# Kernel optimization log

Measured on AMD Instinct MI355X. Metric: run time of the kernel, lower is better.

Reference implementation:

```python
import jax, jax.numpy as jnp
import numpy as np
import math

V, D, L, H, T, B = 32000, 1024, 4, 16, 2048, 1
HD = D // H
EPS = 1e-5

def _pos_encoding(T, D):
    pos = jnp.arange(T, dtype=jnp.float32)[:, None]                      # [T,1]
    div = jnp.exp(jnp.arange(0, D, 2, dtype=jnp.float32) * (-math.log(10000.0) / D))
    ang = pos * div                                                      # [T,D/2]
    pe = jnp.zeros((T, D), dtype=jnp.float32)
    pe = pe.at[:, 0::2].set(jnp.sin(ang)).at[:, 1::2].set(jnp.cos(ang))
    return pe

def _layernorm(x, g, b):
    mu = jnp.mean(x, axis=-1, keepdims=True)
    var = jnp.mean(jnp.square(x - mu), axis=-1, keepdims=True)
    return (x - mu) * jax.lax.rsqrt(var + EPS) * g + b

def setup_inputs() -> dict:
    key = jax.random.key(0)
    ks = jax.random.split(key, 16)
    s = 0.02
    inp = {
        'idx': jax.random.randint(ks[0], (B, T), 0, V),
        'embed': jax.random.normal(ks[1], (V, D), jnp.float32) * s,
        'Wq': jax.random.normal(ks[2], (L, D, D), jnp.float32) * s,
        'Wk': jax.random.normal(ks[3], (L, D, D), jnp.float32) * s,
        'Wv': jax.random.normal(ks[4], (L, D, D), jnp.float32) * s,
        'Wo': jax.random.normal(ks[5], (L, D, D), jnp.float32) * s,
        'bq': jnp.zeros((L, D), jnp.float32),
        'bk': jnp.zeros((L, D), jnp.float32),
        'bv': jnp.zeros((L, D), jnp.float32),
        'bo': jnp.zeros((L, D), jnp.float32),
        'ln1_g': jnp.ones((L, D), jnp.float32), 'ln1_b': jnp.zeros((L, D), jnp.float32),
        'ln2_g': jnp.ones((L, D), jnp.float32), 'ln2_b': jnp.zeros((L, D), jnp.float32),
        'w1': jax.random.normal(ks[6], (L, D, 4 * D), jnp.float32) * s,
        'b1': jnp.zeros((L, 4 * D), jnp.float32),
        'w2': jax.random.normal(ks[7], (L, 4 * D, D), jnp.float32) * s,
        'b2': jnp.zeros((L, D), jnp.float32),
        'lnf_g': jnp.ones((D,), jnp.float32), 'lnf_b': jnp.zeros((D,), jnp.float32),
        'head_w': jax.random.normal(ks[8], (D, V), jnp.float32) * s,
    }
    return inp

def _forward(idx, embed, Wq, Wk, Wv, Wo, bq, bk, bv, bo,
             ln1_g, ln1_b, ln2_g, ln2_b, w1, b1, w2, b2, lnf_g, lnf_b, head_w):
    Bs, Ts = idx.shape
    x = embed[idx] + _pos_encoding(Ts, embed.shape[1])[None]            # [B,T,D]
    causal = jnp.tril(jnp.ones((Ts, Ts), dtype=bool))                   # [T,T]
    scale = 1.0 / math.sqrt(HD)

    def block(x, p):
        wq, wk, wv, wo, q_b, k_b, v_b, o_b, g1, be1, g2, be2, fw1, fb1, fw2, fb2 = p
        h = _layernorm(x, g1, be1)
        q = (h @ wq + q_b).reshape(Bs, Ts, H, HD)
        k = (h @ wk + k_b).reshape(Bs, Ts, H, HD)
        v = (h @ wv + v_b).reshape(Bs, Ts, H, HD)
        att = jnp.einsum('bthd,bshd->bhts', q, k) * scale               # [B,H,T,T]
        att = jnp.where(causal, att, -jnp.inf)
        att = jax.nn.softmax(att, axis=-1)
        o = jnp.einsum('bhts,bshd->bthd', att, v).reshape(Bs, Ts, -1)
        x = x + (o @ wo + o_b)
        h2 = _layernorm(x, g2, be2)
        ff = jax.nn.gelu(h2 @ fw1 + fb1, approximate=False) @ fw2 + fb2
        x = x + ff
        return x, None

    params = (Wq, Wk, Wv, Wo, bq, bk, bv, bo, ln1_g, ln1_b, ln2_g, ln2_b, w1, b1, w2, b2)
    x, _ = jax.lax.scan(block, x, params)
    x = _layernorm(x, lnf_g, lnf_b)
    return x @ head_w                                                   # [B,T,V]

def reference(idx, embed, Wq, Wk, Wv, Wo, bq, bk, bv, bo,
              ln1_g, ln1_b, ln2_g, ln2_b, w1, b1, w2, b2, lnf_g, lnf_b, head_w):
    return _forward(idx, embed, Wq, Wk, Wv, Wo, bq, bk, bv, bo,
                    ln1_g, ln1_b, ln2_g, ln2_b, w1, b1, w2, b2, lnf_g, lnf_b, head_w)
```

## Files before the change

kernel.cpp:

```cpp
#include <hip/hip_runtime.h>
#include <cstdint>

using u16 = unsigned short;
using u32 = unsigned int;
typedef __bf16  bf16x8 __attribute__((ext_vector_type(8)));
typedef float   f32x4  __attribute__((ext_vector_type(4)));
typedef float   f32x16 __attribute__((ext_vector_type(16)));

__device__ __forceinline__ u16 f2b(float x) {
    u32 u = __builtin_bit_cast(u32, x);
    u = (u + 0x7fffu + ((u >> 16) & 1u)) >> 16;
    return (u16)u;
}

__device__ __forceinline__ f32x4 mfma16(bf16x8 a, bf16x8 b, f32x4 c) {
    return __builtin_amdgcn_mfma_f32_16x16x32_bf16(a, b, c, 0, 0, 0);
}
__device__ __forceinline__ f32x16 mfma32(bf16x8 a, bf16x8 b, f32x16 c) {
    return __builtin_amdgcn_mfma_f32_32x32x16_bf16(a, b, c, 0, 0, 0);
}

__device__ __forceinline__ void gload16(const void* g, void* lds) {
    auto gp = (__attribute__((address_space(1))) void*)(uintptr_t)g;
    auto lp = (__attribute__((address_space(3))) void*)(uintptr_t)lds;
    __builtin_amdgcn_global_load_lds(gp, lp, 16, 0, 0);
}

__device__ __forceinline__ int2 swz_bmbn(int nbm) {
    const int nwg = gridDim.x, orig = blockIdx.x;
    const int q = nwg >> 3, r = nwg & 7;
    const int xcd = orig & 7, lin = orig >> 3;
    const int id = (xcd < r ? xcd * (q + 1) : r * (q + 1) + (xcd - r) * q) + lin;
    return make_int2(id % nbm, id / nbm);
}

template <int BM, int KC, int EPI>
__global__ __launch_bounds__(BM == 256 ? 512 : 256, 2) void gemm_deep_k(
    const u16* __restrict__ A, int lda, const u16* __restrict__ Bt, int ldb,
    const float* __restrict__ bias, float* __restrict__ outf,
    u16* __restrict__ outb, int N, int nbm, int sk, long long sOut)
{
    constexpr int NW    = (BM == 256) ? 8 : 4;
    constexpr int WCOLS = (BM == 256) ? 4 : 2;
    constexpr int MF    = BM / 32;
    constexpr int NF    = 4;
    constexpr int SLOT  = BM * 32;
    constexpr int HALF  = (BM / 2) * 32;
    constexpr int H     = KC >> 5;
    constexpr int RPG   = (MF + NF) / 4;
    constexpr int MPG   = (MF * NF) / 4;

    __shared__ __align__(16) u16 lsA[4][SLOT];
    __shared__ __align__(16) u16 lsB[4][SLOT];

    const int s = blockIdx.y;
    A  += (size_t)s * sk;
    Bt += (size_t)s * sk;
    if (EPI == 4) outf += (size_t)s * sOut;

    const int2 bb = swz_bmbn(nbm);
    const int m0 = bb.x * BM, n0 = bb.y * BM;
    const int tid = threadIdx.x;
    const int w = tid >> 6, lane = tid & 63;
    const int wr = (w / WCOLS) * (MF * 16), wc = (w % WCOLS) * 64;
    const int lr = lane & 15, lg = lane >> 4;
    const int rsw = (lg ^ ((lr >> 1) & 3)) * 8;

    const int trow = tid >> 2;
    const int ksw8 = ((tid & 3) ^ ((tid >> 3) & 3)) * 8;
    const u16* aA = A  + (size_t)(m0 + trow) * lda + ksw8;
    const u16* aB = Bt + (size_t)(n0 + trow) * ldb + ksw8;
    u16* dA = &lsA[0][0] + trow * 32 + (tid & 3) * 8;
    u16* dB = &lsB[0][0] + trow * 32 + (tid & 3) * 8;

    f32x4 acc[MF][NF] = {};

    auto stage = [&](int h) {
        const int sl = h & 3;
        const int koff = h * 32;
        gload16(aA + koff,                          dA + sl * SLOT);
        gload16(aA + koff + (size_t)(BM / 2) * lda, dA + sl * SLOT + HALF);
        gload16(aB + koff,                          dB + sl * SLOT);
        gload16(aB + koff + (size_t)(BM / 2) * ldb, dB + sl * SLOT + HALF);
    };

    bf16x8 ra0[MF], rb0[NF], ra1[MF], rb1[NF];
    auto lreadAll = [&](bf16x8* af, bf16x8* bf, int h) {
        const int sl = h & 3;
#pragma unroll
        for (int m = 0; m < MF; m++)
            af[m] = *(const bf16x8*)&lsA[sl][(wr + m * 16 + lr) * 32 + rsw];
#pragma unroll
        for (int n = 0; n < NF; n++)
            bf[n] = *(const bf16x8*)&lsB[sl][(wc + n * 16 + lr) * 32 + rsw];
    };

    auto body = [&](int h, bf16x8* aC, bf16x8* bC, bf16x8* aN, bf16x8* bN) {
        if (h + 3 < H) stage(h + 3);
        __builtin_amdgcn_sched_barrier(0);
        asm volatile("s_waitcnt lgkmcnt(0)" ::: "memory");
        const int rem = H - 1 - h;
        if (rem >= 3)      asm volatile("s_waitcnt vmcnt(8)" ::: "memory");
        else if (rem == 2) asm volatile("s_waitcnt vmcnt(4)" ::: "memory");
        else if (rem == 1) asm volatile("s_waitcnt vmcnt(0)" ::: "memory");
        __builtin_amdgcn_s_barrier();
        __builtin_amdgcn_sched_barrier(0);
        const int sl1 = (h + 1) & 3;
        const bool doRead = (h + 1 < H);
#pragma unroll
        for (int g = 0; g < 4; ++g) {
            if (doRead) {
#pragma unroll
                for (int t = g * RPG; t < (g + 1) * RPG; ++t) {
                    if (t < MF) aN[t]      = *(const bf16x8*)&lsA[sl1][(wr + t * 16 + lr) * 32 + rsw];
                    else        bN[t - MF] = *(const bf16x8*)&lsB[sl1][(wc + (t - MF) * 16 + lr) * 32 + rsw];
                }
            }
            __builtin_amdgcn_sched_barrier(0);
            __builtin_amdgcn_s_setprio(1);
#pragma unroll
            for (int i = g * MPG; i < (g + 1) * MPG; ++i)
                acc[i / NF][i % NF] = mfma16(aC[i / NF], bC[i % NF], acc[i / NF][i % NF]);
            __builtin_amdgcn_s_setprio(0);
            __builtin_amdgcn_sched_barrier(0);
        }
    };

    stage(0); stage(1); stage(2);
    asm volatile("s_waitcnt vmcnt(8)" ::: "memory");
    __builtin_amdgcn_s_barrier();
    lreadAll(ra0, rb0, 0);

#pragma unroll
    for (int h = 0; h < H; h += 2) {
        body(h,     ra0, rb0, ra1, rb1);
        body(h + 1, ra1, rb1, ra0, rb0);
    }

#pragma unroll
    for (int n = 0; n < NF; n++) {
        const int gc = n0 + wc + n * 16 + lr;
        float bv = 0.f;
        if constexpr (EPI == 0 || EPI == 1) bv = bias[gc];
#pragma unroll
        for (int m = 0; m < MF; m++) {
            const int grb = m0 + wr + m * 16 + lg * 4;
#pragma unroll
            for (int r = 0; r < 4; r++) {
                float v = acc[m][n][r] + bv;
                if constexpr (EPI == 1) v = 0.5f * v * (1.f + erff(v * 0.70710678118654752f));
                const size_t o = (size_t)(grb + r) * N + gc;
                if constexpr (EPI == 3 || EPI == 4) outf[o] = v;
                else                                outb[o] = f2b(v);
            }
        }
    }
}

__global__ __launch_bounds__(256) void reduce_ln_k(
    const float* __restrict__ pbuf, int S,
    const float* __restrict__ bias,
    float* __restrict__ x,
    const float* __restrict__ g, const float* __restrict__ bln,
    u16* __restrict__ hb)
{
    __shared__ float red[8];
    const int row = blockIdx.x, tid = threadIdx.x;
    const int w = tid >> 6, lane = tid & 63;
    const size_t base = (size_t)row * 256 + tid;
    float4 v = ((const float4*)x)[base];
    for (int s = 0; s < S; ++s) {
        const float4 p = ((const float4*)pbuf)[(size_t)s * 524288 + base];
        v.x += p.x; v.y += p.y; v.z += p.z; v.w += p.w;
    }
    const float4 bb = ((const float4*)bias)[tid];
    v.x += bb.x; v.y += bb.y; v.z += bb.z; v.w += bb.w;
    ((float4*)x)[base] = v;

    float s1 = v.x + v.y + v.z + v.w;
#pragma unroll
    for (int d = 1; d < 64; d <<= 1) s1 += __shfl_xor(s1, d);
    if (lane == 0) red[w] = s1;
    __syncthreads();
    const float mu = (red[0] + red[1] + red[2] + red[3]) * (1.f / 1024.f);
    const float d0 = v.x - mu, d1 = v.y - mu, d2 = v.z - mu, d3 = v.w - mu;
    float s2 = d0 * d0 + d1 * d1 + d2 * d2 + d3 * d3;
#pragma unroll
    for (int d = 1; d < 64; d <<= 1) s2 += __shfl_xor(s2, d);
    if (lane == 0) red[4 + w] = s2;
    __syncthreads();
    const float var = (red[4] + red[5] + red[6] + red[7]) * (1.f / 1024.f);
    const float rs = rsqrtf(var + 1e-5f);
    const float4 gv = ((const float4*)g)[tid];
    const float4 bv = ((const float4*)bln)[tid];
    u32 p0 = (u32)f2b(d0 * rs * gv.x + bv.x) | ((u32)f2b(d1 * rs * gv.y + bv.y) << 16);
    u32 p1 = (u32)f2b(d2 * rs * gv.z + bv.z) | ((u32)f2b(d3 * rs * gv.w + bv.w) << 16);
    ((uint2*)(hb + (size_t)row * 1024))[tid] = make_uint2(p0, p1);
}

__global__ __launch_bounds__(256) void flash_attn_k(
    const u16* __restrict__ qkv, const u16* __restrict__ vT, u16* __restrict__ out)
{
    constexpr int DS = 3072, T = 2048;
    __shared__ float mrg[2][64][32];
    __shared__ float msh[2][32], lsh[2][32];
    __shared__ u16   sbuf[2][32 * 68];
    const int w = threadIdx.x >> 6, lane = threadIdx.x & 63;
    const int lq = lane & 31, hi = lane >> 5;
    const int hoff = blockIdx.y * 64;
    const int pair = w >> 1, par = w & 1;
    const int qt = (pair == 0) ? blockIdx.x : 63 - blockIdx.x;
    const int q0 = qt * 32;
    const int qg = q0 + lq;

    const u16* qp = qkv + (size_t)qg * DS + hoff;
    const u16* kp = qkv + 1024 + hoff;

    bf16x8 qf[4];
#pragma unroll
    for (int d = 0; d < 4; d++)
        qf[d] = *(const bf16x8*)(qp + d * 16 + hi * 8);

    f32x16 o0 = {}, o1 = {};
    float m_r = -1e30f, l_r = 0.f;

    const int ntiles = (qt >> 1) + 1;
    for (int t = par; t < ntiles; t += 2) {
        const int kv0 = t * 64;
        f32x16 s0 = {}, s1 = {};
        {
            const u16* kb0 = kp + (size_t)(kv0 + lq) * DS + hi * 8;
            const u16* kb1 = kb0 + (size_t)32 * DS;
#pragma unroll
            for (int d = 0; d < 4; d++) {
                s0 = mfma32(*(const bf16x8*)(kb0 + d * 16), qf[d], s0);
                s1 = mfma32(*(const bf16x8*)(kb1 + d * 16), qf[d], s1);
            }
        }
        float p[32];
        float mx = -1e30f;
#pragma unroll
        for (int r = 0; r < 16; r++) {
            const int kvl = (r & 3) + 8 * (r >> 2) + 4 * hi;
            float v0 = (kv0 + kvl      <= qg) ? s0[r] * 0.125f : -1e30f;
            float v1 = (kv0 + 32 + kvl <= qg) ? s1[r] * 0.125f : -1e30f;
            p[r] = v0; p[16 + r] = v1;
            mx = fmaxf(mx, fmaxf(v0, v1));
        }
        mx = fmaxf(mx, __shfl_xor(mx, 32));
        const float mn = fmaxf(m_r, mx);
        const float alpha = __expf(m_r - mn);
        m_r = mn;
        float ls = 0.f;
#pragma unroll
        for (int i = 0; i < 32; i++) { p[i] = __expf(p[i] - mn); ls += p[i]; }
        ls += __shfl_xor(ls, 32);
        l_r = l_r * alpha + ls;
#pragma unroll
        for (int r = 0; r < 16; r++) { o0[r] *= alpha; o1[r] *= alpha; }
#pragma unroll
        for (int sub = 0; sub < 2; sub++) {
            u32 pw[8], x[8];
#pragma unroll
            for (int i = 0; i < 8; i++)
                pw[i] = (u32)f2b(p[sub * 16 + 2 * i]) | ((u32)f2b(p[sub * 16 + 2 * i + 1]) << 16);
#pragma unroll
            for (int i = 0; i < 8; i++) x[i] = __shfl_xor(pw[i], 32);
            u32 b0[4], b1[4];
            b0[0] = hi ? x[2]  : pw[0];  b0[1] = hi ? x[3]  : pw[1];
            b0[2] = hi ? pw[2] : x[0];   b0[3] = hi ? pw[3] : x[1];
            b1[0] = hi ? x[6]  : pw[4];  b1[1] = hi ? x[7]  : pw[5];
            b1[2] = hi ? pw[6] : x[4];   b1[3] = hi ? pw[7] : x[5];
            bf16x8 B0 = __builtin_bit_cast(bf16x8, *(const uint4*)b0);
            bf16x8 B1 = __builtin_bit_cast(bf16x8, *(const uint4*)b1);
            const u16* vb = vT + (size_t)(hoff + lq) * T + kv0 + sub * 32 + hi * 8;
            o0 = mfma32(*(const bf16x8*)vb, B0, o0);
            o0 = mfma32(*(const bf16x8*)(vb + 16), B1, o0);
            const u16* vb1 = vb + (size_t)32 * T;
            o1 = mfma32(*(const bf16x8*)vb1, B0, o1);
            o1 = mfma32(*(const bf16x8*)(vb1 + 16), B1, o1);
        }
    }

    __syncthreads();
    if (par == 0) {
#pragma unroll
        for (int r = 0; r < 16; r++) {
            const int d = (r & 3) + 8 * (r >> 2) + 4 * hi;
            mrg[pair][d][lq]      = o0[r];
            mrg[pair][d + 32][lq] = o1[r];
        }
        if (hi == 0) { msh[pair][lq] = m_r; lsh[pair][lq] = l_r; }
    }
    __syncthreads();
    if (par == 1) {
        const float m0v = msh[pair][lq], l0v = lsh[pair][lq];
        const float M = fmaxf(m0v, m_r);
        const float f0 = __expf(m0v - M), f1 = __expf(m_r - M);
        const float linv = 1.f / (l0v * f0 + l_r * f1);
        u32* sb = (u32*)sbuf[pair];
#pragma unroll
        for (int r = 0; r < 16; r += 2) {
            const int d = (r & 3) + 8 * (r >> 2) + 4 * hi;
            float va = (mrg[pair][d][lq] * f0 + o0[r] * f1) * linv;
            float vb = (mrg[pair][d + 1][lq] * f0 + o0[r + 1] * f1) * linv;
            sb[lq * 34 + (d >> 1)] = (u32)f2b(va) | ((u32)f2b(vb) << 16);
            float vc = (mrg[pair][d + 32][lq] * f0 + o1[r] * f1) * linv;
            float vd = (mrg[pair][d + 33][lq] * f0 + o1[r + 1] * f1) * linv;
            sb[lq * 34 + ((d + 32) >> 1)] = (u32)f2b(vc) | ((u32)f2b(vd) << 16);
        }
#pragma unroll
        for (int ps = 0; ps < 8; ps++) {
            const int row = ps * 4 + (lane >> 4);
            const uint2 v = *(const uint2*)&sbuf[pair][row * 68 + (lane & 15) * 4];
            *(uint2*)(out + (size_t)(q0 + row) * 1024 + hoff + (lane & 15) * 4) = v;
        }
    }
}

__global__ __launch_bounds__(256) void transpose_cvt_k(
    const float* __restrict__ src, u16* __restrict__ dst, int K, int N,
    long long srcLS, long long dstLS)
{
    __shared__ float tile[32][33];
    src += (size_t)blockIdx.z * srcLS;
    dst += (size_t)blockIdx.z * dstLS;
    const int n0 = blockIdx.x * 32, k0 = blockIdx.y * 32;
    const int tx = threadIdx.x & 31, ty = threadIdx.x >> 5;
#pragma unroll
    for (int r = 0; r < 32; r += 8)
        tile[ty + r][tx] = src[(size_t)(k0 + ty + r) * N + n0 + tx];
    __syncthreads();
#pragma unroll
    for (int r = 0; r < 32; r += 8)
        dst[(size_t)(n0 + ty + r) * K + k0 + tx] = f2b(tile[tx][ty + r]);
}

__global__ __launch_bounds__(256) void transpose_u16_k(
    const u16* __restrict__ src, u16* __restrict__ dst, int R, int C, int srcStride)
{
    __shared__ u16 tile[32][33];
    const int c0 = blockIdx.x * 32, r0 = blockIdx.y * 32;
    const int tx = threadIdx.x & 31, ty = threadIdx.x >> 5;
#pragma unroll
    for (int r = 0; r < 32; r += 8)
        tile[ty + r][tx] = src[(size_t)(r0 + ty + r) * srcStride + c0 + tx];
    __syncthreads();
#pragma unroll
    for (int r = 0; r < 32; r += 8)
        dst[(size_t)(c0 + ty + r) * R + r0 + tx] = tile[tx][ty + r];
}

__global__ __launch_bounds__(256) void concat_bias_k(
    const float* __restrict__ bq, const float* __restrict__ bk,
    const float* __restrict__ bv, float* __restrict__ bcat)
{
    const int l = blockIdx.y;
    const int j = blockIdx.x * 256 + threadIdx.x;
    float v;
    if (j < 1024)      v = bq[l * 1024 + j];
    else if (j < 2048) v = bk[l * 1024 + j - 1024];
    else               v = bv[l * 1024 + j - 2048];
    bcat[l * 3072 + j] = v;
}

__global__ __launch_bounds__(256) void embed_pos_k(
    const int* __restrict__ idx, const float* __restrict__ emb, float* __restrict__ x)
{
    const int t = blockIdx.x, tid = threadIdx.x;
    const int tok = idx[t];
    float4 e = ((const float4*)(emb + (size_t)tok * 1024))[tid];
    const int d0 = tid * 4;
    const float c = -0.0089944730195080f;
    const float a0 = (float)t * expf((float)d0 * c);
    const float a1 = (float)t * expf((float)(d0 + 2) * c);
    e.x += sinf(a0); e.y += cosf(a0); e.z += sinf(a1); e.w += cosf(a1);
    ((float4*)(x + (size_t)t * 1024))[tid] = e;
}

__global__ __launch_bounds__(256) void layernorm_k(
    const float* __restrict__ x, const float* __restrict__ g,
    const float* __restrict__ b, u16* __restrict__ out)
{
    __shared__ float red[8];
    const int row = blockIdx.x, tid = threadIdx.x;
    const int w = tid >> 6, lane = tid & 63;
    const float4 v = ((const float4*)(x + (size_t)row * 1024))[tid];
    float s = v.x + v.y + v.z + v.w;
#pragma unroll
    for (int d = 1; d < 64; d <<= 1) s += __shfl_xor(s, d);
    if (lane == 0) red[w] = s;
    __syncthreads();
    const float mu = (red[0] + red[1] + red[2] + red[3]) * (1.f / 1024.f);
    const float d0 = v.x - mu, d1 = v.y - mu, d2 = v.z - mu, d3 = v.w - mu;
    float s2 = d0 * d0 + d1 * d1 + d2 * d2 + d3 * d3;
#pragma unroll
    for (int d = 1; d < 64; d <<= 1) s2 += __shfl_xor(s2, d);
    if (lane == 0) red[4 + w] = s2;
    __syncthreads();
    const float var = (red[4] + red[5] + red[6] + red[7]) * (1.f / 1024.f);
    const float rs = rsqrtf(var + 1e-5f);
    const float4 gv = ((const float4*)g)[tid];
    const float4 bv = ((const float4*)b)[tid];
    u32 p0 = (u32)f2b(d0 * rs * gv.x + bv.x) | ((u32)f2b(d1 * rs * gv.y + bv.y) << 16);
    u32 p1 = (u32)f2b(d2 * rs * gv.z + bv.z) | ((u32)f2b(d3 * rs * gv.w + bv.w) << 16);
    ((uint2*)(out + (size_t)row * 1024))[tid] = make_uint2(p0, p1);
}

extern "C" void kernel_launch(void* const* d_in, const int* in_sizes, int n_in,
                              void* d_out, int out_size, void* d_ws, size_t ws_size,
                              hipStream_t stream)
{
    const int*   idx   = (const int*)  d_in[0];
    const float* embed = (const float*)d_in[1];
    const float* Wq    = (const float*)d_in[2];
    const float* Wk    = (const float*)d_in[3];
    const float* Wv    = (const float*)d_in[4];
    const float* Wo    = (const float*)d_in[5];
    const float* bq    = (const float*)d_in[6];
    const float* bk    = (const float*)d_in[7];
    const float* bv    = (const float*)d_in[8];
    const float* bo    = (const float*)d_in[9];
    const float* ln1g  = (const float*)d_in[10];
    const float* ln1b  = (const float*)d_in[11];
    const float* ln2g  = (const float*)d_in[12];
    const float* ln2b  = (const float*)d_in[13];
    const float* w1    = (const float*)d_in[14];
    const float* b1    = (const float*)d_in[15];
    const float* w2    = (const float*)d_in[16];
    const float* b2    = (const float*)d_in[17];
    const float* lnfg  = (const float*)d_in[18];
    const float* lnfb  = (const float*)d_in[19];
    const float* headw = (const float*)d_in[20];

    char* ws = (char*)d_ws;
    auto alloc = [&](size_t bytes) {
        char* p = ws;
        ws += (bytes + 255) & ~(size_t)255;
        return p;
    };
    u16*   qkvT = (u16*)alloc((size_t)4 * 3072 * 1024 * 2);
    u16*   WoT  = (u16*)alloc((size_t)4 * 1024 * 1024 * 2);
    u16*   w1T  = (u16*)alloc((size_t)4 * 1024 * 4096 * 2);
    u16*   w2T  = (u16*)alloc((size_t)4 * 1024 * 4096 * 2);
    u16*   hT   = (u16*)alloc((size_t)32000 * 1024 * 2);
    float* bcat = (float*)alloc((size_t)4 * 3072 * 4);
    float* x    = (float*)alloc((size_t)2048 * 1024 * 4);
    u16*   hb   = (u16*)alloc((size_t)2048 * 1024 * 2);
    u16*   qkvb = (u16*)alloc((size_t)2048 * 3072 * 2);
    u16*   vTb  = (u16*)alloc((size_t)2048 * 1024 * 2);
    u16*   ab   = (u16*)alloc((size_t)2048 * 1024 * 2);
    u16*   ff   = (u16*)alloc((size_t)2048 * 4096 * 2);
    float* pbuf = (float*)d_out;

    transpose_cvt_k<<<dim3(32, 32, 4),  256, 0, stream>>>(Wq, qkvT,            1024, 1024, 1048576, 3145728);
    transpose_cvt_k<<<dim3(32, 32, 4),  256, 0, stream>>>(Wk, qkvT + 1048576,  1024, 1024, 1048576, 3145728);
    transpose_cvt_k<<<dim3(32, 32, 4),  256, 0, stream>>>(Wv, qkvT + 2097152,  1024, 1024, 1048576, 3145728);
    transpose_cvt_k<<<dim3(32, 32, 4),  256, 0, stream>>>(Wo, WoT,             1024, 1024, 1048576, 1048576);
    transpose_cvt_k<<<dim3(128, 32, 4), 256, 0, stream>>>(w1, w1T,             1024, 4096, 4194304, 4194304);
    transpose_cvt_k<<<dim3(32, 128, 4), 256, 0, stream>>>(w2, w2T,             4096, 1024, 4194304, 4194304);
    transpose_cvt_k<<<dim3(1000, 32, 1), 256, 0, stream>>>(headw, hT,          1024, 32000, 0, 0);
    concat_bias_k<<<dim3(12, 4), 256, 0, stream>>>(bq, bk, bv, bcat);

    embed_pos_k<<<dim3(2048), 256, 0, stream>>>(idx, embed, x);
    layernorm_k<<<dim3(2048), 256, 0, stream>>>(x, ln1g, ln1b, hb);

    for (int l = 0; l < 4; ++l) {
        gemm_deep_k<128, 1024, 0><<<dim3(384), 256, 0, stream>>>(
            hb, 1024, qkvT + (size_t)l * 3145728, 1024,
            bcat + l * 3072, nullptr, qkvb, 3072, 16, 0, 0);
        transpose_u16_k<<<dim3(32, 64), 256, 0, stream>>>(qkvb + 2048, vTb, 2048, 1024, 3072);
        flash_attn_k<<<dim3(32, 16), 256, 0, stream>>>(qkvb, vTb, ab);
        gemm_deep_k<128, 512, 4><<<dim3(128, 2), 256, 0, stream>>>(
            ab, 1024, WoT + (size_t)l * 1048576, 1024,
            nullptr, pbuf, nullptr, 1024, 16, 512, 2097152);
        reduce_ln_k<<<dim3(2048), 256, 0, stream>>>(pbuf, 2, bo + l * 1024, x,
                                                    ln2g + l * 1024, ln2b + l * 1024, hb);
        gemm_deep_k<128, 1024, 1><<<dim3(512), 256, 0, stream>>>(
            hb, 1024, w1T + (size_t)l * 4194304, 1024,
            b1 + l * 4096, nullptr, ff, 4096, 16, 0, 0);
        gemm_deep_k<128, 1024, 4><<<dim3(128, 4), 256, 0, stream>>>(
            ff, 4096, w2T + (size_t)l * 4194304, 4096,
            nullptr, pbuf, nullptr, 1024, 16, 1024, 2097152);
        const float* ng = (l < 3) ? (ln1g + (l + 1) * 1024) : lnfg;
        const float* nb = (l < 3) ? (ln1b + (l + 1) * 1024) : lnfb;
        reduce_ln_k<<<dim3(2048), 256, 0, stream>>>(pbuf, 4, b2 + l * 1024, x, ng, nb, hb);
    }
    gemm_deep_k<256, 1024, 3><<<dim3(1000), 512, 0, stream>>>(
        hb, 1024, hT, 1024, nullptr, (float*)d_out, nullptr, 32000, 8, 0, 0);
}
```

Before: 983.4 us.

## Fuse V transpose into QKV GEMM epilogue, vectorize weight transposes, nontemporal logits

The QKV projection GEMM gains a new epilogue mode that writes the V columns a second time, transposed, into the vT buffer, so the separate transpose_u16 kernel can be dropped. The weight transpose-and-convert kernel now uses float4 loads and 128-wide tiles with packed 8-byte bf16 stores, which cuts the block count and the number of memory transactions. The final logits GEMM writes with nontemporal stores to avoid polluting the cache. The fused transposed store is scattered with a 2048-element stride, so it may coalesce poorly and slow the QKV epilogue.

```diff
diff --git a/kernel.cpp b/kernel.cpp
--- a/kernel.cpp
+++ b/kernel.cpp
@@ -38,9 +38,9 @@
 __global__ __launch_bounds__(BM == 256 ? 512 : 256, 2) void gemm_deep_k(
     const u16* __restrict__ A, int lda, const u16* __restrict__ Bt, int ldb,
     const float* __restrict__ bias, float* __restrict__ outf,
-    u16* __restrict__ outb, int N, int nbm, int sk, long long sOut)
-{
-    constexpr int NW    = (BM == 256) ? 8 : 4;
+    u16* __restrict__ outb, int N, int nbm, int sk, long long sOut,
+    u16* __restrict__ out2)
+{
     constexpr int WCOLS = (BM == 256) ? 4 : 2;
     constexpr int MF    = BM / 32;
     constexpr int NF    = 4;
@@ -141,7 +141,7 @@
     for (int n = 0; n < NF; n++) {
         const int gc = n0 + wc + n * 16 + lr;
         float bv = 0.f;
-        if constexpr (EPI == 0 || EPI == 1) bv = bias[gc];
+        if constexpr (EPI == 0 || EPI == 1 || EPI == 5) bv = bias[gc];
 #pragma unroll
         for (int m = 0; m < MF; m++) {
             const int grb = m0 + wr + m * 16 + lg * 4;
@@ -150,8 +150,16 @@
                 float v = acc[m][n][r] + bv;
                 if constexpr (EPI == 1) v = 0.5f * v * (1.f + erff(v * 0.70710678118654752f));
                 const size_t o = (size_t)(grb + r) * N + gc;
-                if constexpr (EPI == 3 || EPI == 4) outf[o] = v;
-                else                                outb[o] = f2b(v);
+                if constexpr (EPI == 3)      __builtin_nontemporal_store(v, &outf[o]);
+                else if constexpr (EPI == 4) outf[o] = v;
+                else {
+                    const u16 bvv = f2b(v);
+                    outb[o] = bvv;
+                    if constexpr (EPI == 5) {
+                        if (gc >= 2048)
+                            out2[(size_t)(gc - 2048) * 2048 + grb + r] = bvv;
+                    }
+                }
             }
         }
     }
@@ -322,33 +330,28 @@
     const float* __restrict__ src, u16* __restrict__ dst, int K, int N,
     long long srcLS, long long dstLS)
 {
-    __shared__ float tile[32][33];
+    __shared__ float tf[32][132];
     src += (size_t)blockIdx.z * srcLS;
     dst += (size_t)blockIdx.z * dstLS;
-    const int n0 = blockIdx.x * 32, k0 = blockIdx.y * 32;
-    const int tx = threadIdx.x & 31, ty = threadIdx.x >> 5;
-#pragma unroll
-    for (int r = 0; r < 32; r += 8)
-        tile[ty + r][tx] = src[(size_t)(k0 + ty + r) * N + n0 + tx];
-    __syncthreads();
-#pragma unroll
-    for (int r = 0; r < 32; r += 8)
-        dst[(size_t)(n0 + ty + r) * K + k0 + tx] = f2b(tile[tx][ty + r]);
-}
-
-__global__ __launch_bounds__(256) void transpose_u16_k(
-    const u16* __restrict__ src, u16* __restrict__ dst, int R, int C, int srcStride)
-{
-    __shared__ u16 tile[32][33];
-    const int c0 = blockIdx.x * 32, r0 = blockIdx.y * 32;
-    const int tx = threadIdx.x & 31, ty = threadIdx.x >> 5;
-#pragma unroll
-    for (int r = 0; r < 32; r += 8)
-        tile[ty + r][tx] = src[(size_t)(r0 + ty + r) * srcStride + c0 + tx];
-    __syncthreads();
-#pragma unroll
-    for (int r = 0; r < 32; r += 8)
-        dst[(size_t)(c0 + ty + r) * R + r0 + tx] = tile[tx][ty + r];
+    const int n0 = blockIdx.x * 128, k0 = blockIdx.y * 32;
+    const int tid = threadIdx.x;
+    const int tn = tid & 31, tk = tid >> 5;
+#pragma unroll
+    for (int p = 0; p < 4; ++p) {
+        const int k = tk + p * 8;
+        const float4 v = *(const float4*)&src[(size_t)(k0 + k) * N + n0 + tn * 4];
+        *(float4*)&tf[k][tn * 4] = v;
+    }
+    __syncthreads();
+    const int kq = (tid & 7) * 4;
+    const int tn2 = tid >> 3;
+#pragma unroll
+    for (int w = 0; w < 4; ++w) {
+        const int n = tn2 + w * 32;
+        const u32 lo = (u32)f2b(tf[kq + 0][n]) | ((u32)f2b(tf[kq + 1][n]) << 16);
+        const u32 hi = (u32)f2b(tf[kq + 2][n]) | ((u32)f2b(tf[kq + 3][n]) << 16);
+        *(uint2*)&dst[(size_t)(n0 + n) * K + k0 + kq] = make_uint2(lo, hi);
+    }
 }
 
 __global__ __launch_bounds__(256) void concat_bias_k(
@@ -453,39 +456,38 @@
     u16*   ff   = (u16*)alloc((size_t)2048 * 4096 * 2);
     float* pbuf = (float*)d_out;
 
-    transpose_cvt_k<<<dim3(32, 32, 4),  256, 0, stream>>>(Wq, qkvT,            1024, 1024, 1048576, 3145728);
-    transpose_cvt_k<<<dim3(32, 32, 4),  256, 0, stream>>>(Wk, qkvT + 1048576,  1024, 1024, 1048576, 3145728);
-    transpose_cvt_k<<<dim3(32, 32, 4),  256, 0, stream>>>(Wv, qkvT + 2097152,  1024, 1024, 1048576, 3145728);
-    transpose_cvt_k<<<dim3(32, 32, 4),  256, 0, stream>>>(Wo, WoT,             1024, 1024, 1048576, 1048576);
-    transpose_cvt_k<<<dim3(128, 32, 4), 256, 0, stream>>>(w1, w1T,             1024, 4096, 4194304, 4194304);
-    transpose_cvt_k<<<dim3(32, 128, 4), 256, 0, stream>>>(w2, w2T,             4096, 1024, 4194304, 4194304);
-    transpose_cvt_k<<<dim3(1000, 32, 1), 256, 0, stream>>>(headw, hT,          1024, 32000, 0, 0);
+    transpose_cvt_k<<<dim3(8, 32, 4),   256, 0, stream>>>(Wq, qkvT,            1024, 1024, 1048576, 3145728);
+    transpose_cvt_k<<<dim3(8, 32, 4),   256, 0, stream>>>(Wk, qkvT + 1048576,  1024, 1024, 1048576, 3145728);
+    transpose_cvt_k<<<dim3(8, 32, 4),   256, 0, stream>>>(Wv, qkvT + 2097152,  1024, 1024, 1048576, 3145728);
+    transpose_cvt_k<<<dim3(8, 32, 4),   256, 0, stream>>>(Wo, WoT,             1024, 1024, 1048576, 1048576);
+    transpose_cvt_k<<<dim3(32, 32, 4),  256, 0, stream>>>(w1, w1T,             1024, 4096, 4194304, 4194304);
+    transpose_cvt_k<<<dim3(8, 128, 4),  256, 0, stream>>>(w2, w2T,             4096, 1024, 4194304, 4194304);
+    transpose_cvt_k<<<dim3(250, 32, 1), 256, 0, stream>>>(headw, hT,           1024, 32000, 0, 0);
     concat_bias_k<<<dim3(12, 4), 256, 0, stream>>>(bq, bk, bv, bcat);
 
     embed_pos_k<<<dim3(2048), 256, 0, stream>>>(idx, embed, x);
     layernorm_k<<<dim3(2048), 256, 0, stream>>>(x, ln1g, ln1b, hb);
 
     for (int l = 0; l < 4; ++l) {
-        gemm_deep_k<128, 1024, 0><<<dim3(384), 256, 0, stream>>>(
+        gemm_deep_k<128, 1024, 5><<<dim3(384), 256, 0, stream>>>(
             hb, 1024, qkvT + (size_t)l * 3145728, 1024,
-            bcat + l * 3072, nullptr, qkvb, 3072, 16, 0, 0);
-        transpose_u16_k<<<dim3(32, 64), 256, 0, stream>>>(qkvb + 2048, vTb, 2048, 1024, 3072);
+            bcat + l * 3072, nullptr, qkvb, 3072, 16, 0, 0, vTb);
         flash_attn_k<<<dim3(32, 16), 256, 0, stream>>>(qkvb, vTb, ab);
         gemm_deep_k<128, 512, 4><<<dim3(128, 2), 256, 0, stream>>>(
             ab, 1024, WoT + (size_t)l * 1048576, 1024,
-            nullptr, pbuf, nullptr, 1024, 16, 512, 2097152);
+            nullptr, pbuf, nullptr, 1024, 16, 512, 2097152, nullptr);
         reduce_ln_k<<<dim3(2048), 256, 0, stream>>>(pbuf, 2, bo + l * 1024, x,
                                                     ln2g + l * 1024, ln2b + l * 1024, hb);
         gemm_deep_k<128, 1024, 1><<<dim3(512), 256, 0, stream>>>(
             hb, 1024, w1T + (size_t)l * 4194304, 1024,
-            b1 + l * 4096, nullptr, ff, 4096, 16, 0, 0);
+            b1 + l * 4096, nullptr, ff, 4096, 16, 0, 0, nullptr);
         gemm_deep_k<128, 1024, 4><<<dim3(128, 4), 256, 0, stream>>>(
             ff, 4096, w2T + (size_t)l * 4194304, 4096,
-            nullptr, pbuf, nullptr, 1024, 16, 1024, 2097152);
+            nullptr, pbuf, nullptr, 1024, 16, 1024, 2097152, nullptr);
         const float* ng = (l < 3) ? (ln1g + (l + 1) * 1024) : lnfg;
         const float* nb = (l < 3) ? (ln1b + (l + 1) * 1024) : lnfb;
         reduce_ln_k<<<dim3(2048), 256, 0, stream>>>(pbuf, 4, b2 + l * 1024, x, ng, nb, hb);
     }
     gemm_deep_k<256, 1024, 3><<<dim3(1000), 512, 0, stream>>>(
-        hb, 1024, hT, 1024, nullptr, (float*)d_out, nullptr, 32000, 8, 0, 0);
-}
+        hb, 1024, hT, 1024, nullptr, (float*)d_out, nullptr, 32000, 8, 0, 0, nullptr);
+}
```

New measurement: 1.014 ms. 1.03x slower.
